# Kernel tuning notes

Hardware: AMD Instinct MI355X
Metric: run time of the kernel (lower is better)

The kernel has to match this reference:

```python
import jax, jax.numpy as jnp
import numpy as np

B, N = 1, 512
C_S, C_Z, C_HID, H, P_Q, P_V = 384, 128, 16, 12, 4, 8
W_C = (2.0 / (9.0 * P_Q)) ** 0.5
W_L = (1.0 / 3.0) ** 0.5
F_IN = H * C_Z + H * C_HID + H * P_V * 3 + H * P_V  # 2112


def setup_inputs() -> dict:
    key = jax.random.key(0)
    ks = jax.random.split(key, 14)
    s_i = jax.random.normal(ks[0], (B, N, C_S), jnp.float32)
    z_ij = jax.random.normal(ks[1], (B, N, N, C_Z), jnp.float32)
    # proper rotation matrices via QR so invert_apply is a true rigid inverse
    rot, _ = jnp.linalg.qr(jax.random.normal(ks[2], (B, N, 3, 3), jnp.float32))
    trans = jax.random.normal(ks[3], (B, N, 3), jnp.float32)
    sc = lambda fan: 1.0 / np.sqrt(fan)
    Wq = jax.random.normal(ks[4], (C_S, H, C_HID), jnp.float32) * sc(C_S)
    Wk = jax.random.normal(ks[5], (C_S, H, C_HID), jnp.float32) * sc(C_S)
    Wv = jax.random.normal(ks[6], (C_S, H, C_HID), jnp.float32) * sc(C_S)
    Wqp = jax.random.normal(ks[7], (C_S, H, P_Q, 3), jnp.float32) * sc(C_S)
    Wkp = jax.random.normal(ks[8], (C_S, H, P_Q, 3), jnp.float32) * sc(C_S)
    Wvp = jax.random.normal(ks[9], (C_S, H, P_V, 3), jnp.float32) * sc(C_S)
    Wb = jax.random.normal(ks[10], (C_Z, H), jnp.float32) * sc(C_Z)
    gamma = jax.random.normal(ks[11], (H,), jnp.float32)
    Wf = jax.random.normal(ks[12], (F_IN, C_S), jnp.float32) * sc(F_IN)
    bf = jnp.zeros((C_S,), jnp.float32)
    return {"s_i": s_i, "z_ij": z_ij, "rot": rot, "trans": trans,
            "Wq": Wq, "Wk": Wk, "Wv": Wv, "Wqp": Wqp, "Wkp": Wkp, "Wvp": Wvp,
            "Wb": Wb, "gamma": gamma, "Wf": Wf, "bf": bf}


def _apply(rot, trans, p):
    # rigid transform per residue: R_i @ p + t_i ; p: (B,N,H,P,3)
    return jnp.einsum('bimn,bihpn->bihpm', rot, p) + trans[:, :, None, None, :]


def reference(s_i, z_ij, rot, trans, Wq, Wk, Wv, Wqp, Wkp, Wvp, Wb, gamma, Wf, bf):
    q = jnp.einsum('bic,chd->bihd', s_i, Wq)            # (B,N,H,C_HID)
    k = jnp.einsum('bic,chd->bihd', s_i, Wk)
    v = jnp.einsum('bic,chd->bihd', s_i, Wv)
    qp = jnp.einsum('bic,chpx->bihpx', s_i, Wqp)        # (B,N,H,Pq,3)
    kp = jnp.einsum('bic,chpx->bihpx', s_i, Wkp)
    vp = jnp.einsum('bic,chpx->bihpx', s_i, Wvp)        # (B,N,H,Pv,3)
    b_ij = jnp.einsum('bijc,ch->bijh', z_ij, Wb)        # pair bias (B,N,N,H)

    qp_g = _apply(rot, trans, qp)
    kp_g = _apply(rot, trans, kp)
    # squared global point distances, summed over points: (B,N,N,H)
    d2 = jnp.sum((qp_g[:, :, None] - kp_g[:, None]) ** 2, axis=(-1, -2))

    qk = jnp.einsum('bihd,bjhd->bijh', q, k) * (1.0 / np.sqrt(C_HID))
    logits = W_L * (qk + b_ij - (W_C * 0.5) * gamma * d2)
    a = jax.nn.softmax(logits, axis=2)                  # softmax over j

    o_pair = jnp.einsum('bijh,bijc->bihc', a, z_ij)     # (B,N,H,C_Z)
    o_sc = jnp.einsum('bijh,bjhd->bihd', a, v)          # (B,N,H,C_HID)
    vp_g = _apply(rot, trans, vp)
    o_pt_g = jnp.einsum('bijh,bjhpx->bihpx', a, vp_g)   # (B,N,H,Pv,3)
    # invert_apply at residue i: R_i^T @ (x - t_i)
    o_pt = jnp.einsum('bimn,bihpm->bihpn', rot, o_pt_g - trans[:, :, None, None, :])
    o_norm = jnp.sqrt(jnp.sum(o_pt ** 2, axis=-1) + 1e-12)  # (B,N,H,Pv)

    feat = jnp.concatenate([o_pair.reshape(B, N, -1), o_sc.reshape(B, N, -1),
                            o_pt.reshape(B, N, -1), o_norm.reshape(B, N, -1)], axis=-1)
    return feat @ Wf + bf
```

## Files before the change

kernel.cpp:

```cpp
#include <hip/hip_runtime.h>
#include <hip/hip_bf16.h>
#include <math.h>

#define Nn    512
#define CS    384
#define CZ    128
#define CH    16
#define Hh    12
#define PQ    4
#define PV    8
#define NCOL  1152
#define FIN   2112

#define W_C   0.23570226039551584f
#define W_L   0.5773502691896258f

typedef unsigned short ushort_t;
typedef unsigned int uint_t;
typedef __attribute__((ext_vector_type(8))) short bf16x8;
typedef __attribute__((ext_vector_type(4))) float f32x4;

#define OFF_P      0u
#define OFF_MQ     589824u
#define OFF_MK     595968u
#define OFF_VT     602112u
#define OFF_VPT    651264u
#define OFF_S16    1830912u
#define OFF_WCT    1929216u
#define OFF_WFT    2150400u
#define OFF_F16    2555904u
#define OFF_PP     3145728u
#define OFF_VFRAG  5328896u
#define OFF_EXT    5451776u
#define OFF_EKB    21755904u
#define OFF_EQB    21854208u
#define OFF_WBF    21952512u

__device__ inline ushort_t f2bf(float f) {
  __hip_bfloat16 h = __float2bfloat16(f);
  return *reinterpret_cast<ushort_t*>(&h);
}
__device__ inline float bf2f(ushort_t u) {
  unsigned int x = ((unsigned int)u) << 16;
  return __uint_as_float(x);
}

__global__ __launch_bounds__(384) void k_conv(
    const float* __restrict__ s, const float* __restrict__ Wq,
    const float* __restrict__ Wk, const float* __restrict__ Wv,
    const float* __restrict__ Wqp, const float* __restrict__ Wkp,
    const float* __restrict__ Wvp, const float* __restrict__ Wf,
    ushort_t* __restrict__ s16, ushort_t* __restrict__ WcatT,
    ushort_t* __restrict__ WfT) {
  int b = blockIdx.x;
  if (b < 512) {
    int idx = b * 384 + threadIdx.x;
    s16[idx] = f2bf(s[idx]);
  } else if (b < 1664) {
    int col = b - 512, k = threadIdx.x;
    float v;
    if      (col < 192)  v = Wq [k * 192 + col];
    else if (col < 384)  v = Wk [k * 192 + col - 192];
    else if (col < 576)  v = Wv [k * 192 + col - 384];
    else if (col < 720)  v = Wqp[k * 144 + col - 576];
    else if (col < 864)  v = Wkp[k * 144 + col - 720];
    else                 v = Wvp[k * 288 + col - 864];
    WcatT[(size_t)col * CS + k] = f2bf(v);
  } else {
    int o = b - 1664;
    for (int f = threadIdx.x; f < FIN; f += 384)
      WfT[(size_t)o * FIN + f] = f2bf(Wf[(size_t)f * CS + o]);
  }
}

__global__ __launch_bounds__(64) void k_projm(
    const ushort_t* __restrict__ s16, const ushort_t* __restrict__ WcatT,
    float* __restrict__ P) {
  int colt = blockIdx.x;
  int i0 = blockIdx.y * 16;
  int l = threadIdx.x;
  int cl = l & 15, lk = l >> 4;
  f32x4 acc = {0.f, 0.f, 0.f, 0.f};
  const ushort_t* arow = s16 + (size_t)(i0 + cl) * CS;
  const ushort_t* brow = WcatT + (size_t)(colt * 16 + cl) * CS;
#pragma unroll
  for (int kk = 0; kk < 12; ++kk) {
    bf16x8 a = *(const bf16x8*)(arow + kk * 32 + lk * 8);
    bf16x8 b = *(const bf16x8*)(brow + kk * 32 + lk * 8);
    acc = __builtin_amdgcn_mfma_f32_16x16x32_bf16(a, b, acc, 0, 0, 0);
  }
#pragma unroll
  for (int r = 0; r < 4; ++r)
    P[(size_t)(i0 + lk * 4 + r) * NCOL + colt * 16 + cl] = acc[r];
}

__global__ __launch_bounds__(64) void k_prep(
    const float* __restrict__ P, const float* __restrict__ rot,
    const float* __restrict__ trans, const float* __restrict__ gamma,
    ushort_t* __restrict__ eqb, ushort_t* __restrict__ ekb,
    float* __restrict__ mq, float* __restrict__ mk,
    ushort_t* __restrict__ vT, ushort_t* __restrict__ vpT) {
  int gid = blockIdx.x * 64 + threadIdx.x;
  int i = gid / Hh, h = gid % Hh;
  const float* Pi = P + (size_t)i * NCOL;
  float R[9], T[3];
#pragma unroll
  for (int m = 0; m < 9; ++m) R[m] = rot[i * 9 + m];
#pragma unroll
  for (int m = 0; m < 3; ++m) T[m] = trans[i * 3 + m];
  float cg = W_C * gamma[h];

  ushort_t* eq = eqb + (size_t)gid * 32;
  ushort_t* ek = ekb + (size_t)gid * 32;
#pragma unroll
  for (int d = 0; d < CH; ++d) eq[d] = f2bf(Pi[h * CH + d] * 0.25f);
#pragma unroll
  for (int d = 0; d < CH; ++d) ek[d] = f2bf(Pi[192 + h * CH + d]);
  float sq = 0.f, sk = 0.f;
#pragma unroll
  for (int p = 0; p < PQ; ++p) {
    float x = Pi[576 + h * 12 + p * 3 + 0];
    float y = Pi[576 + h * 12 + p * 3 + 1];
    float zc = Pi[576 + h * 12 + p * 3 + 2];
    float gx = R[0] * x + R[1] * y + R[2] * zc + T[0];
    float gy = R[3] * x + R[4] * y + R[5] * zc + T[1];
    float gz = R[6] * x + R[7] * y + R[8] * zc + T[2];
    eq[16 + p * 3 + 0] = f2bf(cg * gx);
    eq[16 + p * 3 + 1] = f2bf(cg * gy);
    eq[16 + p * 3 + 2] = f2bf(cg * gz);
    sq += gx * gx + gy * gy + gz * gz;
  }
#pragma unroll
  for (int p = 0; p < PQ; ++p) {
    float x = Pi[720 + h * 12 + p * 3 + 0];
    float y = Pi[720 + h * 12 + p * 3 + 1];
    float zc = Pi[720 + h * 12 + p * 3 + 2];
    float gx = R[0] * x + R[1] * y + R[2] * zc + T[0];
    float gy = R[3] * x + R[4] * y + R[5] * zc + T[1];
    float gz = R[6] * x + R[7] * y + R[8] * zc + T[2];
    ek[16 + p * 3 + 0] = f2bf(gx);
    ek[16 + p * 3 + 1] = f2bf(gy);
    ek[16 + p * 3 + 2] = f2bf(gz);
    sk += gx * gx + gy * gy + gz * gz;
  }
#pragma unroll
  for (int d = 28; d < 32; ++d) { eq[d] = 0; ek[d] = 0; }
  mq[gid] = -0.5f * cg * sq;
  mk[gid] = -0.5f * cg * sk;

#pragma unroll
  for (int d = 0; d < CH; ++d)
    vT[(size_t)(h * CH + d) * Nn + i] = f2bf(Pi[384 + h * CH + d]);
#pragma unroll
  for (int p = 0; p < PV; ++p) {
    float x = Pi[864 + h * 24 + p * 3 + 0];
    float y = Pi[864 + h * 24 + p * 3 + 1];
    float zc = Pi[864 + h * 24 + p * 3 + 2];
    vpT[(size_t)(h * 24 + p * 3 + 0) * Nn + i] = f2bf(R[0] * x + R[1] * y + R[2] * zc + T[0]);
    vpT[(size_t)(h * 24 + p * 3 + 1) * Nn + i] = f2bf(R[3] * x + R[4] * y + R[5] * zc + T[1]);
    vpT[(size_t)(h * 24 + p * 3 + 2) * Nn + i] = f2bf(R[6] * x + R[7] * y + R[8] * zc + T[2]);
  }
}

__global__ __launch_bounds__(256) void k_wbfrag(
    const float* __restrict__ Wb, ushort_t* __restrict__ wbf) {
  int t = threadIdx.x;
  int kk = t >> 6, l = t & 63;
  int h = l & 15, lk = l >> 4;
#pragma unroll
  for (int e = 0; e < 8; ++e) {
    int c = kk * 32 + lk * 8 + e;
    wbf[t * 8 + e] = (h < Hh) ? f2bf(Wb[c * Hh + h]) : (ushort_t)0;
  }
}

__global__ __launch_bounds__(64) void k_vfrag(
    const ushort_t* __restrict__ vT, const ushort_t* __restrict__ vpT,
    ushort_t* __restrict__ vfrag) {
  int tt = blockIdx.x;
  int jb = blockIdx.y;
  int l = threadIdx.x;
  int cl = l & 15, lk = l >> 4;
  const ushort_t* src = (tt < 12)
      ? vT  + (size_t)(tt * 16 + cl) * Nn
      : vpT + (size_t)((tt - 12) * 16 + cl) * Nn;
  bf16x8 v = *(const bf16x8*)(src + jb * 32 + lk * 8);
  *(bf16x8*)(vfrag + (((size_t)tt * 16 + jb) * 64 + l) * 8) = v;
}

__global__ __launch_bounds__(768) void k_ext(
    const ushort_t* __restrict__ eqb, const ushort_t* __restrict__ ekb,
    const float* __restrict__ mk, float* __restrict__ ext) {
  int it = blockIdx.x, jt = blockIdx.y;
  int tid = threadIdx.x;
  int l = tid & 63, h = tid >> 6;
  int cl = l & 15, lk = l >> 4;
  bf16x8 a = *(const bf16x8*)(eqb + ((size_t)(it * 16 + cl) * Hh + h) * 32 + lk * 8);
  bf16x8 b = *(const bf16x8*)(ekb + ((size_t)(jt * 16 + cl) * Hh + h) * 32 + lk * 8);
  f32x4 dl = {0.f, 0.f, 0.f, 0.f};
  dl = __builtin_amdgcn_mfma_f32_16x16x32_bf16(a, b, dl, 0, 0, 0);
  float mkv = mk[(jt * 16 + cl) * Hh + h];
  float* erow = ext + ((size_t)h * Nn + it * 16 + lk * 4) * Nn + jt * 16 + cl;
#pragma unroll
  for (int r = 0; r < 4; ++r) erow[(size_t)r * Nn] = dl[r] + mkv;
}

__global__ __launch_bounds__(512, 4) void k_fused8(
    const float* __restrict__ z, const ushort_t* __restrict__ wbf,
    const float* __restrict__ ext, const ushort_t* __restrict__ vfrag,
    float* __restrict__ pp) {
  __shared__ float smemf[19728];
  char*   ztc  = (char*)smemf;
  float*  extb = smemf + 16384;
  char*   pB   = (char*)(smemf + 16384);
  float*  mb   = smemf + 19456;
  float*  lb   = smemf + 19584;
  float*  Mv   = smemf + 19712;

  int i = blockIdx.x, half = blockIdx.y, tid = threadIdx.x;
  int l = tid & 63, w = tid >> 6;
  int cl = l & 15, lk = l >> 4;
  int j0b = half * 256;
  float* po = pp + ((size_t)i * 2 + half) * 2048;
  int swz = (cl & 7) << 4;

  const float4* zg4 = (const float4*)(z + ((size_t)i * Nn + j0b) * CZ);
  float4 xv0 = zg4[0 * 512 + tid],  xv1 = zg4[1 * 512 + tid];
  float4 xv2 = zg4[2 * 512 + tid],  xv3 = zg4[3 * 512 + tid];
  float4 xv4 = zg4[4 * 512 + tid],  xv5 = zg4[5 * 512 + tid];
  float4 xv6 = zg4[6 * 512 + tid],  xv7 = zg4[7 * 512 + tid];
  float4 xv8 = zg4[8 * 512 + tid],  xv9 = zg4[9 * 512 + tid];
  float4 xv10 = zg4[10 * 512 + tid], xv11 = zg4[11 * 512 + tid];
  float4 xv12 = zg4[12 * 512 + tid], xv13 = zg4[13 * 512 + tid];
  float4 xv14 = zg4[14 * 512 + tid], xv15 = zg4[15 * 512 + tid];
  float ev[6];
#pragma unroll
  for (int q = 0; q < 6; ++q) {
    int idx = q * 512 + tid;
    ev[q] = ext[((size_t)(idx >> 8) * Nn + i) * Nn + j0b + (idx & 255)];
  }

#define STORE_ZT(it_, xv_) { \
    int idx = (it_) * 512 + tid; \
    int row = idx >> 5, c4 = idx & 31; \
    uint2 pk; \
    pk.x = (uint_t)f2bf(xv_.x) | ((uint_t)f2bf(xv_.y) << 16); \
    pk.y = (uint_t)f2bf(xv_.z) | ((uint_t)f2bf(xv_.w) << 16); \
    *(uint2*)&ztc[row * 256 + ((c4 * 8) ^ ((row & 7) << 4))] = pk; }
  STORE_ZT(0, xv0)   STORE_ZT(1, xv1)   STORE_ZT(2, xv2)   STORE_ZT(3, xv3)
  STORE_ZT(4, xv4)   STORE_ZT(5, xv5)   STORE_ZT(6, xv6)   STORE_ZT(7, xv7)
  STORE_ZT(8, xv8)   STORE_ZT(9, xv9)   STORE_ZT(10, xv10) STORE_ZT(11, xv11)
  STORE_ZT(12, xv12) STORE_ZT(13, xv13) STORE_ZT(14, xv14) STORE_ZT(15, xv15)
#undef STORE_ZT
#pragma unroll
  for (int q = 0; q < 6; ++q) {
    int idx = q * 512 + tid;
    extb[(idx & 255) * 12 + (idx >> 8)] = ev[q];
  }
  __syncthreads();

  bf16x8 wbreg[4];
#pragma unroll
  for (int kk = 0; kk < 4; ++kk)
    wbreg[kk] = *(const bf16x8*)&wbf[(kk * 64 + l) * 8];

  float v[2][4];
#pragma unroll
  for (int cg = 0; cg < 2; ++cg) {
    int jloc = w * 32 + cg * 16 + cl;
    f32x4 dl = {0.f, 0.f, 0.f, 0.f};
#pragma unroll
    for (int kk = 0; kk < 4; ++kk) {
      bf16x8 a = *(const bf16x8*)&ztc[jloc * 256 + ((kk * 64 + lk * 16) ^ ((cl & 7) << 4))];
      dl = __builtin_amdgcn_mfma_f32_16x16x32_bf16(a, wbreg[kk], dl, 0, 0, 0);
    }
    if (cl < Hh) {
#pragma unroll
      for (int r = 0; r < 4; ++r)
        v[cg][r] = W_L * (dl[r] + extb[(w * 32 + cg * 16 + lk * 4 + r) * 12 + cl]);
    } else {
#pragma unroll
      for (int r = 0; r < 4; ++r) v[cg][r] = -1e30f;
    }
  }
  __syncthreads();

  float m_w = v[0][0];
#pragma unroll
  for (int cg = 0; cg < 2; ++cg)
#pragma unroll
    for (int r = 0; r < 4; ++r) m_w = fmaxf(m_w, v[cg][r]);
  m_w = fmaxf(m_w, __shfl_xor(m_w, 16));
  m_w = fmaxf(m_w, __shfl_xor(m_w, 32));

  float ps = 0.f;
#pragma unroll
  for (int cg = 0; cg < 2; ++cg) {
    int j = w * 32 + cg * 16 + lk * 4;
    ushort_t p0 = f2bf(__expf(v[cg][0] - m_w));
    ushort_t p1 = f2bf(__expf(v[cg][1] - m_w));
    ushort_t p2 = f2bf(__expf(v[cg][2] - m_w));
    ushort_t p3 = f2bf(__expf(v[cg][3] - m_w));
    ps += bf2f(p0) + bf2f(p1) + bf2f(p2) + bf2f(p3);
    uint2 d;
    d.x = (uint_t)p0 | ((uint_t)p1 << 16);
    d.y = (uint_t)p2 | ((uint_t)p3 << 16);
    *(uint2*)&pB[(cl * 512 + j * 2) ^ swz] = d;
  }
  ps += __shfl_xor(ps, 16);
  ps += __shfl_xor(ps, 32);
  if (lk == 0) { mb[w * 16 + cl] = m_w; lb[w * 16 + cl] = ps; }
  __syncthreads();

  if (tid < 16) {
    float M = mb[tid];
#pragma unroll
    for (int ww = 1; ww < 8; ++ww) M = fmaxf(M, mb[ww * 16 + tid]);
    float L = 0.f;
#pragma unroll
    for (int ww = 0; ww < 8; ++ww) L += lb[ww * 16 + tid] * __expf(mb[ww * 16 + tid] - M);
    Mv[tid] = M;
    po[2016 + tid] = M;
    po[2032 + tid] = L;
  }
  __syncthreads();

  float sf = __expf(m_w - Mv[cl]);
#pragma unroll
  for (int q = 0; q < 2; ++q) {
    int j = w * 32 + lk * 8 + q * 4;
    uint_t off = (uint_t)(cl * 512 + j * 2) ^ swz;
    uint2 d = *(uint2*)&pB[off];
    ushort_t q0 = f2bf(bf2f((ushort_t)(d.x & 0xffff)) * sf);
    ushort_t q1 = f2bf(bf2f((ushort_t)(d.x >> 16)) * sf);
    ushort_t q2 = f2bf(bf2f((ushort_t)(d.y & 0xffff)) * sf);
    ushort_t q3 = f2bf(bf2f((ushort_t)(d.y >> 16)) * sf);
    d.x = (uint_t)q0 | ((uint_t)q1 << 16);
    d.y = (uint_t)q2 | ((uint_t)q3 << 16);
    *(uint2*)&pB[off] = d;
  }
  __syncthreads();

  f32x4 acc[5];
#pragma unroll
  for (int n = 0; n < 5; ++n) acc[n] = (f32x4){0.f, 0.f, 0.f, 0.f};
  bf16x8 vA[4], vB[4];

#define LOADV(buf, kk_) { \
    _Pragma("unroll") \
    for (int n = 1; n < 5; ++n) { \
      int t = w + n * 8; \
      if (t < 38) buf[n - 1] = *(const bf16x8*)(vfrag + \
          (((size_t)(t - 8) * 16 + (half * 8 + (kk_))) * 64 + l) * 8); \
    } }
#define COMPUTE(buf, kk_) { \
    int koff = (kk_) * 32 + lk * 8; \
    bf16x8 af = *(const bf16x8*)&pB[(cl * 512 + koff * 2) ^ swz]; \
    bf16x8 b0; \
    _Pragma("unroll") \
    for (int e = 0; e < 8; ++e) \
      b0[e] = *(const short*)&ztc[(koff + e) * 256 + ((w * 32 + cl * 2) ^ (e << 4))]; \
    acc[0] = __builtin_amdgcn_mfma_f32_16x16x32_bf16(af, b0, acc[0], 0, 0, 0); \
    _Pragma("unroll") \
    for (int n = 1; n < 5; ++n) { \
      int t = w + n * 8; \
      if (t < 38) acc[n] = __builtin_amdgcn_mfma_f32_16x16x32_bf16(af, buf[n - 1], acc[n], 0, 0, 0); \
    } }

  LOADV(vA, 0)
#pragma unroll
  for (int kk = 0; kk < 8; kk += 2) {
    LOADV(vB, kk + 1)
    COMPUTE(vA, kk)
    if (kk < 6) LOADV(vA, kk + 2)
    COMPUTE(vB, kk + 1)
  }
#undef LOADV
#undef COMPUTE

#pragma unroll
  for (int n = 0; n < 5; ++n) {
    int t = w + n * 8;
    if (t < 38) {
      if (t < 8) {
        int c = t * 16 + cl;
#pragma unroll
        for (int r = 0; r < 4; ++r) {
          int h = lk * 4 + r;
          if (h < Hh) po[h * CZ + c] = acc[n][r];
        }
      } else if (t < 20) {
        int h = t - 8;
        if (lk == (h >> 2)) po[1536 + h * CH + cl] = acc[n][h & 3];
      } else {
        int cp = (t - 20) * 16 + cl;
        int h = cp / 24;
        if (lk == (h >> 2)) po[1728 + cp] = acc[n][h & 3];
      }
    }
  }
}

__global__ __launch_bounds__(256) void k_merge(
    const float* __restrict__ pp, const float* __restrict__ rot,
    const float* __restrict__ trans, ushort_t* __restrict__ feat16) {
  __shared__ float a0s[16], a1s[16];
  __shared__ float optg[288];
  int i = blockIdx.x, tid = threadIdx.x;
  const float* p0 = pp + ((size_t)i * 2 + 0) * 2048;
  const float* p1 = pp + ((size_t)i * 2 + 1) * 2048;
  ushort_t* Fi = feat16 + (size_t)i * FIN;

  if (tid < 16) {
    float m0 = p0[2016 + tid], m1 = p1[2016 + tid];
    float M = fmaxf(m0, m1);
    float s0 = __expf(m0 - M), s1 = __expf(m1 - M);
    float L = p0[2032 + tid] * s0 + p1[2032 + tid] * s1;
    float inv = (tid < Hh) ? 1.f / L : 0.f;
    a0s[tid] = s0 * inv;
    a1s[tid] = s1 * inv;
  }
  __syncthreads();

  for (int idx = tid; idx < 1728; idx += 256) {
    int h = (idx < 1536) ? (idx >> 7) : ((idx - 1536) >> 4);
    Fi[idx] = f2bf(p0[idx] * a0s[h] + p1[idx] * a1s[h]);
  }
  for (int idx = tid; idx < 288; idx += 256) {
    int h = idx / 24;
    optg[idx] = p0[1728 + idx] * a0s[h] + p1[1728 + idx] * a1s[h];
  }
  __syncthreads();

  if (tid < 96) {
    int h = tid >> 3, p = tid & 7;
    int cp = h * 24 + p * 3;
    float g0 = optg[cp + 0] - trans[i * 3 + 0];
    float g1 = optg[cp + 1] - trans[i * 3 + 1];
    float g2 = optg[cp + 2] - trans[i * 3 + 2];
    const float* R = rot + i * 9;
    float ss = 0.f;
#pragma unroll
    for (int nn2 = 0; nn2 < 3; ++nn2) {
      float o = R[nn2] * g0 + R[3 + nn2] * g1 + R[6 + nn2] * g2;
      Fi[1728 + cp + nn2] = f2bf(o);
      ss += o * o;
    }
    Fi[2016 + h * 8 + p] = f2bf(sqrtf(ss + 1e-12f));
  }
}

__global__ __launch_bounds__(64) void k_outm(
    const ushort_t* __restrict__ feat16, const ushort_t* __restrict__ WfT,
    const float* __restrict__ bfv, float* __restrict__ out) {
  int ot = blockIdx.x;
  int i0 = blockIdx.y * 16;
  int l = threadIdx.x;
  int cl = l & 15, lk = l >> 4;
  f32x4 acc = {0.f, 0.f, 0.f, 0.f};
  const ushort_t* arow = feat16 + (size_t)(i0 + cl) * FIN;
  const ushort_t* brow = WfT + (size_t)(ot * 16 + cl) * FIN;
#pragma unroll 6
  for (int kk = 0; kk < 66; ++kk) {
    bf16x8 a = *(const bf16x8*)(arow + kk * 32 + lk * 8);
    bf16x8 b = *(const bf16x8*)(brow + kk * 32 + lk * 8);
    acc = __builtin_amdgcn_mfma_f32_16x16x32_bf16(a, b, acc, 0, 0, 0);
  }
  float bias = bfv[ot * 16 + cl];
#pragma unroll
  for (int r = 0; r < 4; ++r)
    out[(size_t)(i0 + lk * 4 + r) * CS + ot * 16 + cl] = acc[r] + bias;
}

extern "C" void kernel_launch(void* const* d_in, const int* in_sizes, int n_in,
                              void* d_out, int out_size, void* d_ws, size_t ws_size,
                              hipStream_t stream) {
  const float* s_i   = (const float*)d_in[0];
  const float* z_ij  = (const float*)d_in[1];
  const float* rot   = (const float*)d_in[2];
  const float* trans = (const float*)d_in[3];
  const float* Wq    = (const float*)d_in[4];
  const float* Wk    = (const float*)d_in[5];
  const float* Wv    = (const float*)d_in[6];
  const float* Wqp   = (const float*)d_in[7];
  const float* Wkp   = (const float*)d_in[8];
  const float* Wvp   = (const float*)d_in[9];
  const float* Wb    = (const float*)d_in[10];
  const float* gamma = (const float*)d_in[11];
  const float* Wf    = (const float*)d_in[12];
  const float* bf    = (const float*)d_in[13];
  float* out = (float*)d_out;

  float* w = (float*)d_ws;
  float*    P     = w + OFF_P;
  float*    mq    = w + OFF_MQ;
  float*    mk    = w + OFF_MK;
  ushort_t* vT    = (ushort_t*)(w + OFF_VT);
  ushort_t* vpT   = (ushort_t*)(w + OFF_VPT);
  ushort_t* s16   = (ushort_t*)(w + OFF_S16);
  ushort_t* WcT   = (ushort_t*)(w + OFF_WCT);
  ushort_t* WfT   = (ushort_t*)(w + OFF_WFT);
  ushort_t* f16   = (ushort_t*)(w + OFF_F16);
  float*    pp    = w + OFF_PP;
  ushort_t* vfrag = (ushort_t*)(w + OFF_VFRAG);
  float*    ext   = w + OFF_EXT;
  ushort_t* ekb   = (ushort_t*)(w + OFF_EKB);
  ushort_t* eqb   = (ushort_t*)(w + OFF_EQB);
  ushort_t* wbf   = (ushort_t*)(w + OFF_WBF);

  k_conv<<<2048, 384, 0, stream>>>(s_i, Wq, Wk, Wv, Wqp, Wkp, Wvp, Wf, s16, WcT, WfT);
  k_projm<<<dim3(72, 32), 64, 0, stream>>>(s16, WcT, P);
  k_prep<<<96, 64, 0, stream>>>(P, rot, trans, gamma, eqb, ekb, mq, mk, vT, vpT);
  k_wbfrag<<<1, 256, 0, stream>>>(Wb, wbf);
  k_vfrag<<<dim3(30, 16), 64, 0, stream>>>(vT, vpT, vfrag);
  k_ext<<<dim3(32, 32), 768, 0, stream>>>(eqb, ekb, mk, ext);
  k_fused8<<<dim3(512, 2), 512, 0, stream>>>(z_ij, wbf, ext, vfrag, pp);
  k_merge<<<512, 256, 0, stream>>>(pp, rot, trans, f16);
  k_outm<<<dim3(24, 32), 64, 0, stream>>>(f16, WfT, bf, out);
}
```

Measured before the change: 96.04 us.

## Fold Wb fragment prep into conversion kernel and split-K the output GEMM

```diff
diff --git a/kernel.cpp b/kernel.cpp
--- a/kernel.cpp
+++ b/kernel.cpp
@@ -50,8 +50,9 @@
     const float* __restrict__ Wk, const float* __restrict__ Wv,
     const float* __restrict__ Wqp, const float* __restrict__ Wkp,
     const float* __restrict__ Wvp, const float* __restrict__ Wf,
+    const float* __restrict__ Wb,
     ushort_t* __restrict__ s16, ushort_t* __restrict__ WcatT,
-    ushort_t* __restrict__ WfT) {
+    ushort_t* __restrict__ WfT, ushort_t* __restrict__ wbf) {
   int b = blockIdx.x;
   if (b < 512) {
     int idx = b * 384 + threadIdx.x;
@@ -66,10 +67,21 @@
     else if (col < 864)  v = Wkp[k * 144 + col - 720];
     else                 v = Wvp[k * 288 + col - 864];
     WcatT[(size_t)col * CS + k] = f2bf(v);
-  } else {
+  } else if (b < 2048) {
     int o = b - 1664;
     for (int f = threadIdx.x; f < FIN; f += 384)
       WfT[(size_t)o * FIN + f] = f2bf(Wf[(size_t)f * CS + o]);
+  } else {
+    int t = threadIdx.x;
+    if (t < 256) {
+      int kk = t >> 6, l = t & 63;
+      int h = l & 15, lk = l >> 4;
+#pragma unroll
+      for (int e = 0; e < 8; ++e) {
+        int c = kk * 32 + lk * 8 + e;
+        wbf[t * 8 + e] = (h < Hh) ? f2bf(Wb[c * Hh + h]) : (ushort_t)0;
+      }
+    }
   }
 }
 
@@ -80,18 +92,21 @@
   int i0 = blockIdx.y * 16;
   int l = threadIdx.x;
   int cl = l & 15, lk = l >> 4;
-  f32x4 acc = {0.f, 0.f, 0.f, 0.f};
+  f32x4 accA = {0.f, 0.f, 0.f, 0.f}, accB = {0.f, 0.f, 0.f, 0.f};
   const ushort_t* arow = s16 + (size_t)(i0 + cl) * CS;
   const ushort_t* brow = WcatT + (size_t)(colt * 16 + cl) * CS;
 #pragma unroll
-  for (int kk = 0; kk < 12; ++kk) {
-    bf16x8 a = *(const bf16x8*)(arow + kk * 32 + lk * 8);
-    bf16x8 b = *(const bf16x8*)(brow + kk * 32 + lk * 8);
-    acc = __builtin_amdgcn_mfma_f32_16x16x32_bf16(a, b, acc, 0, 0, 0);
+  for (int kk = 0; kk < 12; kk += 2) {
+    bf16x8 a0 = *(const bf16x8*)(arow + kk * 32 + lk * 8);
+    bf16x8 b0 = *(const bf16x8*)(brow + kk * 32 + lk * 8);
+    accA = __builtin_amdgcn_mfma_f32_16x16x32_bf16(a0, b0, accA, 0, 0, 0);
+    bf16x8 a1 = *(const bf16x8*)(arow + (kk + 1) * 32 + lk * 8);
+    bf16x8 b1 = *(const bf16x8*)(brow + (kk + 1) * 32 + lk * 8);
+    accB = __builtin_amdgcn_mfma_f32_16x16x32_bf16(a1, b1, accB, 0, 0, 0);
   }
 #pragma unroll
   for (int r = 0; r < 4; ++r)
-    P[(size_t)(i0 + lk * 4 + r) * NCOL + colt * 16 + cl] = acc[r];
+    P[(size_t)(i0 + lk * 4 + r) * NCOL + colt * 16 + cl] = accA[r] + accB[r];
 }
 
 __global__ __launch_bounds__(64) void k_prep(
@@ -159,18 +174,6 @@
     vpT[(size_t)(h * 24 + p * 3 + 0) * Nn + i] = f2bf(R[0] * x + R[1] * y + R[2] * zc + T[0]);
     vpT[(size_t)(h * 24 + p * 3 + 1) * Nn + i] = f2bf(R[3] * x + R[4] * y + R[5] * zc + T[1]);
     vpT[(size_t)(h * 24 + p * 3 + 2) * Nn + i] = f2bf(R[6] * x + R[7] * y + R[8] * zc + T[2]);
-  }
-}
-
-__global__ __launch_bounds__(256) void k_wbfrag(
-    const float* __restrict__ Wb, ushort_t* __restrict__ wbf) {
-  int t = threadIdx.x;
-  int kk = t >> 6, l = t & 63;
-  int h = l & 15, lk = l >> 4;
-#pragma unroll
-  for (int e = 0; e < 8; ++e) {
-    int c = kk * 32 + lk * 8 + e;
-    wbf[t * 8 + e] = (h < Hh) ? f2bf(Wb[c * Hh + h]) : (ushort_t)0;
   }
 }
 
@@ -450,26 +453,48 @@
   }
 }
 
-__global__ __launch_bounds__(64) void k_outm(
+__global__ __launch_bounds__(256) void k_outm2(
     const ushort_t* __restrict__ feat16, const ushort_t* __restrict__ WfT,
     const float* __restrict__ bfv, float* __restrict__ out) {
+  __shared__ f32x4 red[4][64];
   int ot = blockIdx.x;
-  int i0 = blockIdx.y * 16;
-  int l = threadIdx.x;
+  int ib = blockIdx.y;
+  int tid = threadIdx.x;
+  int l = tid & 63, w = tid >> 6;
   int cl = l & 15, lk = l >> 4;
-  f32x4 acc = {0.f, 0.f, 0.f, 0.f};
+  int i0 = ib * 32 + (w >> 1) * 16;
+  int kw = w & 1;
   const ushort_t* arow = feat16 + (size_t)(i0 + cl) * FIN;
   const ushort_t* brow = WfT + (size_t)(ot * 16 + cl) * FIN;
-#pragma unroll 6
-  for (int kk = 0; kk < 66; ++kk) {
+  f32x4 accA = {0.f, 0.f, 0.f, 0.f}, accB = {0.f, 0.f, 0.f, 0.f};
+  int k0 = kw * 33;
+#pragma unroll 4
+  for (int kk = k0; kk < k0 + 32; kk += 2) {
+    bf16x8 a0 = *(const bf16x8*)(arow + kk * 32 + lk * 8);
+    bf16x8 b0 = *(const bf16x8*)(brow + kk * 32 + lk * 8);
+    accA = __builtin_amdgcn_mfma_f32_16x16x32_bf16(a0, b0, accA, 0, 0, 0);
+    bf16x8 a1 = *(const bf16x8*)(arow + (kk + 1) * 32 + lk * 8);
+    bf16x8 b1 = *(const bf16x8*)(brow + (kk + 1) * 32 + lk * 8);
+    accB = __builtin_amdgcn_mfma_f32_16x16x32_bf16(a1, b1, accB, 0, 0, 0);
+  }
+  {
+    int kk = k0 + 32;
     bf16x8 a = *(const bf16x8*)(arow + kk * 32 + lk * 8);
     bf16x8 b = *(const bf16x8*)(brow + kk * 32 + lk * 8);
-    acc = __builtin_amdgcn_mfma_f32_16x16x32_bf16(a, b, acc, 0, 0, 0);
-  }
-  float bias = bfv[ot * 16 + cl];
-#pragma unroll
-  for (int r = 0; r < 4; ++r)
-    out[(size_t)(i0 + lk * 4 + r) * CS + ot * 16 + cl] = acc[r] + bias;
+    accA = __builtin_amdgcn_mfma_f32_16x16x32_bf16(a, b, accA, 0, 0, 0);
+  }
+#pragma unroll
+  for (int r = 0; r < 4; ++r) accA[r] += accB[r];
+  red[w][l] = accA;
+  __syncthreads();
+  if (kw == 0) {
+    f32x4 s = red[w][l];
+    f32x4 o = red[w + 1][l];
+    float bias = bfv[ot * 16 + cl];
+#pragma unroll
+    for (int r = 0; r < 4; ++r)
+      out[(size_t)(i0 + lk * 4 + r) * CS + ot * 16 + cl] = s[r] + o[r] + bias;
+  }
 }
 
 extern "C" void kernel_launch(void* const* d_in, const int* in_sizes, int n_in,
@@ -508,13 +533,13 @@
   ushort_t* eqb   = (ushort_t*)(w + OFF_EQB);
   ushort_t* wbf   = (ushort_t*)(w + OFF_WBF);
 
-  k_conv<<<2048, 384, 0, stream>>>(s_i, Wq, Wk, Wv, Wqp, Wkp, Wvp, Wf, s16, WcT, WfT);
+  k_conv<<<2049, 384, 0, stream>>>(s_i, Wq, Wk, Wv, Wqp, Wkp, Wvp, Wf, Wb,
+                                   s16, WcT, WfT, wbf);
   k_projm<<<dim3(72, 32), 64, 0, stream>>>(s16, WcT, P);
   k_prep<<<96, 64, 0, stream>>>(P, rot, trans, gamma, eqb, ekb, mq, mk, vT, vpT);
-  k_wbfrag<<<1, 256, 0, stream>>>(Wb, wbf);
   k_vfrag<<<dim3(30, 16), 64, 0, stream>>>(vT, vpT, vfrag);
   k_ext<<<dim3(32, 32), 768, 0, stream>>>(eqb, ekb, mk, ext);
   k_fused8<<<dim3(512, 2), 512, 0, stream>>>(z_ij, wbf, ext, vfrag, pp);
   k_merge<<<512, 256, 0, stream>>>(pp, rot, trans, f16);
-  k_outm<<<dim3(24, 32), 64, 0, stream>>>(f16, WfT, bf, out);
-}
+  k_outm2<<<dim3(24, 16), 256, 0, stream>>>(f16, WfT, bf, out);
+}
```

Measured after the change: 94.09 us. 1.02x faster.
